# Optimization experiments

Measured on AMD Instinct MI355X. Metric: run time of the kernel, lower is better.

Reference implementation:

```python
import jax, jax.numpy as jnp
import numpy as np

N_NODES = 100000
D_FEAT = 128
N_EDGES = 1600000


def setup_inputs() -> dict:
    key = jax.random.key(0)
    k1, k2 = jax.random.split(key)
    x = jax.random.normal(k1, (N_NODES, D_FEAT), dtype=jnp.float32)
    edge_index = jax.random.randint(k2, (2, N_EDGES), 0, N_NODES, dtype=jnp.int32)
    return {"x": x, "edge_index": edge_index}


def reference(x, edge_index):
    # flow='source_to_target': i=1 (target), j=0 (source)
    # message = x_j (identity), aggregate = scatter-add into targets, update = identity
    src = edge_index[0]
    dst = edge_index[1]
    msg = x[src]  # [E, d] gather
    out = jax.ops.segment_sum(msg, dst, num_segments=x.shape[0])  # [N, d] scatter-add
    return out
```

## Files before the change

### kernel.cpp

```cpp
#include <hip/hip_runtime.h>

constexpr int N_NODES = 100000;
constexpr int D_FEAT  = 128;
constexpr int N_EDGES = 1600000;

constexpr int SHIFT    = 6;
constexpr int BUCKET_W = 1 << SHIFT;
constexpr int NB       = (N_NODES + BUCKET_W - 1) >> SHIFT;

constexpr int EPB       = 8192;
constexpr int MS_BLOCKS = (N_EDGES + EPB - 1) / EPB;
constexpr int FUSE_GRID = 512;
static_assert(N_EDGES % 4 == 0 && EPB % 4 == 0, "int4 edge loads");

constexpr int      SRC_BITS = 17;
constexpr unsigned SRC_MASK = (1u << SRC_BITS) - 1u;

constexpr int CAP = 1280;
constexpr int SG_THREADS = 512;

typedef unsigned short ushort8 __attribute__((ext_vector_type(8)));
typedef float          floatx4 __attribute__((ext_vector_type(4)));

__device__ inline unsigned short f32_to_bf16_rne(float f)
{
    unsigned u = __float_as_uint(f);
    return (unsigned short)((u + 0x7FFFu + ((u >> 16) & 1u)) >> 16);
}
__device__ inline float bf16_to_f32(unsigned short h)
{
    return __uint_as_float((unsigned)h << 16);
}

__device__ inline int wave_incl_scan(int v)
{
    #pragma unroll
    for (int off = 1; off < 64; off <<= 1) {
        int t = __shfl_up(v, off);
        if ((threadIdx.x & 63) >= off) v += t;
    }
    return v;
}

__device__ inline void convert_span(const float* __restrict__ x,
                                    unsigned short* __restrict__ xh,
                                    long long tid0, long long stride)
{
    const long long nq = ((long long)N_NODES * D_FEAT) >> 2;
    for (long long q = tid0; q < nq; q += stride) {
        float4 v = reinterpret_cast<const float4*>(x)[q];
        ushort4 h;
        h.x = f32_to_bf16_rne(v.x);
        h.y = f32_to_bf16_rne(v.y);
        h.z = f32_to_bf16_rne(v.z);
        h.w = f32_to_bf16_rne(v.w);
        reinterpret_cast<ushort4*>(xh)[q] = h;
    }
}

__global__ void __launch_bounds__(1024) split_convert_kernel(
    const int* __restrict__ src, const int* __restrict__ dst,
    int* __restrict__ cursor, unsigned* __restrict__ coarse,
    const float* __restrict__ x, unsigned short* __restrict__ xh)
{
    if (blockIdx.x >= MS_BLOCKS) {
        convert_span(x, xh,
                     (long long)(blockIdx.x - MS_BLOCKS) * 1024 + threadIdx.x,
                     (long long)(gridDim.x - MS_BLOCKS) * 1024);
        return;
    }

    __shared__ int h[NB], gb[NB], lc[NB];
    const int t = threadIdx.x, blk = blockIdx.x;
    for (int i = t; i < NB; i += 1024) h[i] = 0;
    __syncthreads();

    const int base = blk * EPB;
    const int cnt  = min(EPB, N_EDGES - base);
    const int nq   = cnt >> 2;
    const int4* dst4 = reinterpret_cast<const int4*>(dst + base);
    const int4* src4 = reinterpret_cast<const int4*>(src + base);

    for (int k = t; k < nq; k += 1024) {
        int4 d = dst4[k];
        atomicAdd(&h[d.x >> SHIFT], 1);
        atomicAdd(&h[d.y >> SHIFT], 1);
        atomicAdd(&h[d.z >> SHIFT], 1);
        atomicAdd(&h[d.w >> SHIFT], 1);
    }
    __syncthreads();

    for (int b = t; b < NB; b += 1024) {
        lc[b] = 0;
        gb[b] = (h[b] > 0) ? atomicAdd(&cursor[b], h[b]) : 0;
    }
    __syncthreads();

    for (int k = t; k < nq; k += 1024) {
        int4 d = dst4[k];
        int4 s = src4[k];
        {
            int b = d.x >> SHIFT;
            int pos = gb[b] + atomicAdd(&lc[b], 1);
            if (pos < CAP)
                coarse[(size_t)b * CAP + pos] =
                    ((unsigned)(d.x & (BUCKET_W - 1)) << SRC_BITS) | (unsigned)s.x;
        }
        {
            int b = d.y >> SHIFT;
            int pos = gb[b] + atomicAdd(&lc[b], 1);
            if (pos < CAP)
                coarse[(size_t)b * CAP + pos] =
                    ((unsigned)(d.y & (BUCKET_W - 1)) << SRC_BITS) | (unsigned)s.y;
        }
        {
            int b = d.z >> SHIFT;
            int pos = gb[b] + atomicAdd(&lc[b], 1);
            if (pos < CAP)
                coarse[(size_t)b * CAP + pos] =
                    ((unsigned)(d.z & (BUCKET_W - 1)) << SRC_BITS) | (unsigned)s.z;
        }
        {
            int b = d.w >> SHIFT;
            int pos = gb[b] + atomicAdd(&lc[b], 1);
            if (pos < CAP)
                coarse[(size_t)b * CAP + pos] =
                    ((unsigned)(d.w & (BUCKET_W - 1)) << SRC_BITS) | (unsigned)s.w;
        }
    }
}

__global__ void __launch_bounds__(SG_THREADS) sortgather_kernel(
    const unsigned* __restrict__ coarse, const int* __restrict__ cursor,
    const unsigned short* __restrict__ xh, float* __restrict__ out)
{
    __shared__ unsigned stage[CAP];
    __shared__ int ids[CAP];
    __shared__ int hist[BUCKET_W];
    __shared__ int lcur[BUCKET_W];
    __shared__ int ofs[BUCKET_W + 1];

    const int blk = blockIdx.x, t = threadIdx.x;
    const int node0  = blk << SHIFT;
    const int nn     = min(BUCKET_W, N_NODES - node0);
    const int seglen = min(cursor[blk], CAP);

    if (t < BUCKET_W) hist[t] = 0;
    __syncthreads();

    const unsigned* cb = coarse + (size_t)blk * CAP;
    for (int i = t; i < seglen; i += SG_THREADS) {
        unsigned p = cb[i];
        stage[i] = p;
        atomicAdd(&hist[p >> SRC_BITS], 1);
    }
    __syncthreads();

    if (t < BUCKET_W) {
        int v = hist[t];
        int incl = wave_incl_scan(v);
        ofs[t]  = incl - v;
        lcur[t] = incl - v;
        if (t == BUCKET_W - 1) ofs[BUCKET_W] = incl;
    }
    __syncthreads();

    for (int i = t; i < seglen; i += SG_THREADS) {
        unsigned p = stage[i];
        int pos = atomicAdd(&lcur[p >> SRC_BITS], 1);
        ids[pos] = (int)(p & SRC_MASK);
    }
    __syncthreads();

    const int w    = t >> 6;
    const int lane = t & 63;
    const int u    = lane >> 4;
    const int c    = lane & 15;
    const unsigned short* xb = xh + c * 8;

    const int lend = min((w + 1) * 8, nn);
    for (int ln = w * 8; ln < lend; ++ln) {
        const int beg = ofs[ln];
        const int end = ofs[ln + 1];

        float acc[8] = {0.f, 0.f, 0.f, 0.f, 0.f, 0.f, 0.f, 0.f};

        int e = beg;
        for (; e + 8 <= end; e += 8) {
            int s0 = ids[e + u];
            int s1 = ids[e + 4 + u];
            ushort8 v0 = *reinterpret_cast<const ushort8*>(xb + (size_t)s0 * D_FEAT);
            ushort8 v1 = *reinterpret_cast<const ushort8*>(xb + (size_t)s1 * D_FEAT);
            #pragma unroll
            for (int j = 0; j < 8; ++j)
                acc[j] += bf16_to_f32(v0[j]) + bf16_to_f32(v1[j]);
        }
        if (e + 4 <= end) {
            int s0 = ids[e + u];
            ushort8 v0 = *reinterpret_cast<const ushort8*>(xb + (size_t)s0 * D_FEAT);
            #pragma unroll
            for (int j = 0; j < 8; ++j) acc[j] += bf16_to_f32(v0[j]);
            e += 4;
        }
        const int r = end - e;
        if (u < r) {
            int s0 = ids[e + u];
            ushort8 v0 = *reinterpret_cast<const ushort8*>(xb + (size_t)s0 * D_FEAT);
            #pragma unroll
            for (int j = 0; j < 8; ++j) acc[j] += bf16_to_f32(v0[j]);
        }

        #pragma unroll
        for (int j = 0; j < 8; ++j) {
            acc[j] += __shfl_xor(acc[j], 16);
            acc[j] += __shfl_xor(acc[j], 32);
        }

        if (u == 0) {
            floatx4 a = {acc[0], acc[1], acc[2], acc[3]};
            floatx4 b = {acc[4], acc[5], acc[6], acc[7]};
            float* o = out + (size_t)(node0 + ln) * D_FEAT + c * 8;
            __builtin_nontemporal_store(a, reinterpret_cast<floatx4*>(o));
            __builtin_nontemporal_store(b, reinterpret_cast<floatx4*>(o + 4));
        }
    }
}

__global__ void __launch_bounds__(256) atomic_scatter_kernel(
    const float* __restrict__ x, const int* __restrict__ src,
    const int* __restrict__ dst, float* __restrict__ out)
{
    long long T = (long long)blockIdx.x * blockDim.x + threadIdx.x;
    int edge = (int)(T >> 5), chunk = (int)(T & 31);
    if (edge >= N_EDGES) return;
    int s = src[edge], d = dst[edge];
    const float4 v = *reinterpret_cast<const float4*>(x + (long long)s * D_FEAT + chunk * 4);
    float* o = out + (long long)d * D_FEAT + chunk * 4;
    atomicAdd(o + 0, v.x); atomicAdd(o + 1, v.y);
    atomicAdd(o + 2, v.z); atomicAdd(o + 3, v.w);
}

extern "C" void kernel_launch(void* const* d_in, const int* in_sizes, int n_in,
                              void* d_out, int out_size, void* d_ws, size_t ws_size,
                              hipStream_t stream)
{
    const float* x          = (const float*)d_in[0];
    const int*   edge_index = (const int*)d_in[1];
    const int*   src        = edge_index;
    const int*   dst        = edge_index + N_EDGES;
    float*       out        = (float*)d_out;

    char*  ws       = (char*)d_ws;
    size_t o_cur    = 0;
    size_t o_coarse = (o_cur + (size_t)NB * 4 + 63) & ~(size_t)63;
    size_t o_xh     = (o_coarse + (size_t)NB * CAP * 4 + 63) & ~(size_t)63;
    size_t need     = o_xh + (size_t)N_NODES * D_FEAT * 2;

    int*            cursor = (int*)(ws + o_cur);
    unsigned*       coarse = (unsigned*)(ws + o_coarse);
    unsigned short* xh     = (unsigned short*)(ws + o_xh);

    if (ws_size < need) {
        (void)hipMemsetAsync(out, 0, (size_t)N_NODES * D_FEAT * sizeof(float), stream);
        const long long tt = (long long)N_EDGES * 32;
        atomic_scatter_kernel<<<(int)((tt + 255) / 256), 256, 0, stream>>>(
            x, src, dst, out);
        return;
    }

    (void)hipMemsetAsync(cursor, 0, (size_t)NB * 4, stream);

    split_convert_kernel<<<FUSE_GRID, 1024, 0, stream>>>(
        src, dst, cursor, coarse, x, xh);
    sortgather_kernel<<<NB, SG_THREADS, 0, stream>>>(
        coarse, cursor, xh, out);
}
```

Baseline: 102.6 us.

## Sort bucket edges by source slice and interleave node accumulation for L2 locality

```diff
diff --git a/kernel.cpp b/kernel.cpp
--- a/kernel.cpp
+++ b/kernel.cpp
@@ -16,6 +16,10 @@
 constexpr int      SRC_BITS = 17;
 constexpr unsigned SRC_MASK = (1u << SRC_BITS) - 1u;
 
+constexpr int NS_SHIFT = 13;
+constexpr int NSLICE   = ((N_NODES - 1) >> NS_SHIFT) + 1;
+constexpr int KEYS     = BUCKET_W * 16;
+
 constexpr int CAP = 1280;
 constexpr int SG_THREADS = 512;
 
@@ -40,6 +44,22 @@
         if ((threadIdx.x & 63) >= off) v += t;
     }
     return v;
+}
+
+__device__ inline int block_excl_scan_512(int v, int* wsum)
+{
+    int lane = threadIdx.x & 63, wid = threadIdx.x >> 6;
+    int incl = wave_incl_scan(v);
+    if (lane == 63) wsum[wid] = incl;
+    __syncthreads();
+    if (wid == 0) {
+        int s = (lane < 8) ? wsum[lane] : 0;
+        s = wave_incl_scan(s);
+        if (lane < 8) wsum[lane] = s;
+    }
+    __syncthreads();
+    int woff = (wid > 0) ? wsum[wid - 1] : 0;
+    return incl + woff - v;
 }
 
 __device__ inline void convert_span(const float* __restrict__ x,
@@ -99,53 +119,38 @@
     for (int k = t; k < nq; k += 1024) {
         int4 d = dst4[k];
         int4 s = src4[k];
-        {
-            int b = d.x >> SHIFT;
+        #pragma unroll
+        for (int e = 0; e < 4; ++e) {
+            int dd = (e == 0) ? d.x : (e == 1) ? d.y : (e == 2) ? d.z : d.w;
+            int ss = (e == 0) ? s.x : (e == 1) ? s.y : (e == 2) ? s.z : s.w;
+            int b = dd >> SHIFT;
             int pos = gb[b] + atomicAdd(&lc[b], 1);
-            if (pos < CAP)
-                coarse[(size_t)b * CAP + pos] =
-                    ((unsigned)(d.x & (BUCKET_W - 1)) << SRC_BITS) | (unsigned)s.x;
-        }
-        {
-            int b = d.y >> SHIFT;
-            int pos = gb[b] + atomicAdd(&lc[b], 1);
-            if (pos < CAP)
-                coarse[(size_t)b * CAP + pos] =
-                    ((unsigned)(d.y & (BUCKET_W - 1)) << SRC_BITS) | (unsigned)s.y;
-        }
-        {
-            int b = d.z >> SHIFT;
-            int pos = gb[b] + atomicAdd(&lc[b], 1);
-            if (pos < CAP)
-                coarse[(size_t)b * CAP + pos] =
-                    ((unsigned)(d.z & (BUCKET_W - 1)) << SRC_BITS) | (unsigned)s.z;
-        }
-        {
-            int b = d.w >> SHIFT;
-            int pos = gb[b] + atomicAdd(&lc[b], 1);
-            if (pos < CAP)
-                coarse[(size_t)b * CAP + pos] =
-                    ((unsigned)(d.w & (BUCKET_W - 1)) << SRC_BITS) | (unsigned)s.w;
-        }
-    }
-}
-
-__global__ void __launch_bounds__(SG_THREADS) sortgather_kernel(
+            if (pos < CAP) {
+                unsigned key = ((unsigned)(dd & (BUCKET_W - 1)) << 4) |
+                               (unsigned)(ss >> NS_SHIFT);
+                coarse[(size_t)b * CAP + pos] = (key << SRC_BITS) | (unsigned)ss;
+            }
+        }
+    }
+}
+
+__global__ void __launch_bounds__(SG_THREADS, 4) sortgather_kernel(
     const unsigned* __restrict__ coarse, const int* __restrict__ cursor,
     const unsigned short* __restrict__ xh, float* __restrict__ out)
 {
     __shared__ unsigned stage[CAP];
     __shared__ int ids[CAP];
-    __shared__ int hist[BUCKET_W];
-    __shared__ int lcur[BUCKET_W];
-    __shared__ int ofs[BUCKET_W + 1];
+    __shared__ int hist[KEYS];
+    __shared__ int lcur[KEYS];
+    __shared__ int ofs[KEYS + 1];
+    __shared__ int wsum[8];
 
     const int blk = blockIdx.x, t = threadIdx.x;
     const int node0  = blk << SHIFT;
     const int nn     = min(BUCKET_W, N_NODES - node0);
     const int seglen = min(cursor[blk], CAP);
 
-    if (t < BUCKET_W) hist[t] = 0;
+    for (int i = t; i < KEYS; i += SG_THREADS) hist[i] = 0;
     __syncthreads();
 
     const unsigned* cb = coarse + (size_t)blk * CAP;
@@ -156,13 +161,13 @@
     }
     __syncthreads();
 
-    if (t < BUCKET_W) {
-        int v = hist[t];
-        int incl = wave_incl_scan(v);
-        ofs[t]  = incl - v;
-        lcur[t] = incl - v;
-        if (t == BUCKET_W - 1) ofs[BUCKET_W] = incl;
-    }
+    const int a0 = hist[2 * t], a1 = hist[2 * t + 1];
+    const int ex = block_excl_scan_512(a0 + a1, wsum);
+    ofs[2 * t]      = ex;
+    ofs[2 * t + 1]  = ex + a0;
+    lcur[2 * t]     = ex;
+    lcur[2 * t + 1] = ex + a0;
+    if (t == SG_THREADS - 1) ofs[KEYS] = ex + a0 + a1;
     __syncthreads();
 
     for (int i = t; i < seglen; i += SG_THREADS) {
@@ -178,47 +183,46 @@
     const int c    = lane & 15;
     const unsigned short* xb = xh + c * 8;
 
-    const int lend = min((w + 1) * 8, nn);
-    for (int ln = w * 8; ln < lend; ++ln) {
-        const int beg = ofs[ln];
-        const int end = ofs[ln + 1];
-
-        float acc[8] = {0.f, 0.f, 0.f, 0.f, 0.f, 0.f, 0.f, 0.f};
-
-        int e = beg;
-        for (; e + 8 <= end; e += 8) {
-            int s0 = ids[e + u];
-            int s1 = ids[e + 4 + u];
-            ushort8 v0 = *reinterpret_cast<const ushort8*>(xb + (size_t)s0 * D_FEAT);
-            ushort8 v1 = *reinterpret_cast<const ushort8*>(xb + (size_t)s1 * D_FEAT);
-            #pragma unroll
-            for (int j = 0; j < 8; ++j)
-                acc[j] += bf16_to_f32(v0[j]) + bf16_to_f32(v1[j]);
-        }
-        if (e + 4 <= end) {
-            int s0 = ids[e + u];
-            ushort8 v0 = *reinterpret_cast<const ushort8*>(xb + (size_t)s0 * D_FEAT);
-            #pragma unroll
-            for (int j = 0; j < 8; ++j) acc[j] += bf16_to_f32(v0[j]);
-            e += 4;
-        }
-        const int r = end - e;
-        if (u < r) {
-            int s0 = ids[e + u];
-            ushort8 v0 = *reinterpret_cast<const ushort8*>(xb + (size_t)s0 * D_FEAT);
-            #pragma unroll
-            for (int j = 0; j < 8; ++j) acc[j] += bf16_to_f32(v0[j]);
-        }
-
+    float acc[8][8];
+    #pragma unroll
+    for (int j = 0; j < 8; ++j)
+        #pragma unroll
+        for (int k = 0; k < 8; ++k) acc[j][k] = 0.f;
+
+    for (int s = 0; s < NSLICE; ++s) {
         #pragma unroll
         for (int j = 0; j < 8; ++j) {
-            acc[j] += __shfl_xor(acc[j], 16);
-            acc[j] += __shfl_xor(acc[j], 32);
-        }
-
-        if (u == 0) {
-            floatx4 a = {acc[0], acc[1], acc[2], acc[3]};
-            floatx4 b = {acc[4], acc[5], acc[6], acc[7]};
+            const int key = ((w * 8 + j) << 4) | s;
+            const int beg = ofs[key];
+            const int end = ofs[key + 1];
+            int e = beg;
+            for (; e + 4 <= end; e += 4) {
+                int s0 = ids[e + u];
+                ushort8 v0 = *reinterpret_cast<const ushort8*>(xb + (size_t)s0 * D_FEAT);
+                #pragma unroll
+                for (int k = 0; k < 8; ++k) acc[j][k] += bf16_to_f32(v0[k]);
+            }
+            const int r = end - e;
+            if (u < r) {
+                int s0 = ids[e + u];
+                ushort8 v0 = *reinterpret_cast<const ushort8*>(xb + (size_t)s0 * D_FEAT);
+                #pragma unroll
+                for (int k = 0; k < 8; ++k) acc[j][k] += bf16_to_f32(v0[k]);
+            }
+        }
+    }
+
+    #pragma unroll
+    for (int j = 0; j < 8; ++j) {
+        const int ln = w * 8 + j;
+        #pragma unroll
+        for (int k = 0; k < 8; ++k) {
+            acc[j][k] += __shfl_xor(acc[j][k], 16);
+            acc[j][k] += __shfl_xor(acc[j][k], 32);
+        }
+        if (u == 0 && ln < nn) {
+            floatx4 a = {acc[j][0], acc[j][1], acc[j][2], acc[j][3]};
+            floatx4 b = {acc[j][4], acc[j][5], acc[j][6], acc[j][7]};
             float* o = out + (size_t)(node0 + ln) * D_FEAT + c * 8;
             __builtin_nontemporal_store(a, reinterpret_cast<floatx4*>(o));
             __builtin_nontemporal_store(b, reinterpret_cast<floatx4*>(o + 4));
```

After: 195.1 us. 1.9x slower.
